# Kernel optimization log

Hardware: AMD Instinct MI355X
Metric: run time of the kernel (lower is better)

Reference implementation:

```python
import jax, jax.numpy as jnp
import numpy as np

B, T, C, H, S, M = 4, 4096, 1024, 16, 256, 32
D = C // H  # size_head = 64


def setup_inputs() -> dict:
    key = jax.random.key(0)
    ks = jax.random.split(key, 10)
    scale = 1.0 / (C * C)
    return {
        "x_q": jax.random.normal(ks[0], (B, T, C), dtype=jnp.float32),
        "x_r": jax.random.normal(ks[1], (B, T, C), dtype=jnp.float32),
        "y": jax.random.normal(ks[2], (B, T, C), dtype=jnp.float32),
        "Wi": jax.random.normal(ks[3], (C, C), dtype=jnp.float32) * 0.02,
        "bi": jnp.zeros((C,), jnp.float32),
        "Ws": jax.random.normal(ks[4], (S, D), dtype=jnp.float32) * 0.02,
        "bs": jnp.zeros((S,), jnp.float32),
        "temp": jnp.ones((1, H, 1, 1), jnp.float32) / jnp.sqrt(jnp.float32(D)),
        "w_re": jax.random.uniform(ks[5], (H, D, D, M), dtype=jnp.float32) * scale,
        "w_im": jax.random.uniform(ks[6], (H, D, D, M), dtype=jnp.float32) * scale,
        "Wo": jax.random.normal(ks[7], (C, C), dtype=jnp.float32) * 0.02,
        "bo": jnp.zeros((C,), jnp.float32),
    }


def reference(x_q, x_r, y, Wi, bi, Ws, bs, temp, w_re, w_im, Wo, bo):
    b, t, c = x_q.shape
    d = c // H
    # in_proj -> [B, H, T, D]
    tmp = (x_q @ Wi.T + bi).reshape(b, t, H, d).transpose(0, 2, 1, 3)
    # slice logits [B, H, T, S], scaled by learned temperature
    logits = (tmp @ Ws.T + bs) / temp
    # softmax over tokens (n): slice-attention pooling to S virtual points
    z = jnp.einsum('bhnc,bhns->bhsc', tmp, jax.nn.softmax(logits, axis=-2))
    z = z.transpose(0, 1, 3, 2)  # [B, H, D, S]
    n = z.shape[-1]
    z_fft = jnp.fft.rfft(z)  # [B, H, D, S//2+1]
    w = (w_re + 1j * w_im).astype(z_fft.dtype)
    out_m = jnp.einsum('bhix,hiox->bhox', z_fft[..., :M], w)  # [B, H, D, M]
    out_ft = jnp.zeros((b, H, d, n // 2 + 1), dtype=out_m.dtype).at[..., :M].set(out_m)
    out = jnp.fft.irfft(out_ft, n=n)  # [B, H, D, S]
    out = out.transpose(0, 1, 3, 2)  # [B, H, S, D]
    # softmax over slices (g): scatter back to tokens
    out = jnp.einsum('bhgc,bhng->bhnc', out, jax.nn.softmax(logits, axis=-1))
    out = out.transpose(0, 2, 1, 3).reshape(b, t, c)  # merge heads
    return out @ Wo.T + bo
```

## Files before the change

### kernel.cpp

```cpp
#include <hip/hip_runtime.h>
#include <hip/hip_bf16.h>

typedef __attribute__((ext_vector_type(8))) _Float16 half8;
typedef __attribute__((ext_vector_type(4))) _Float16 half4;
typedef __attribute__((ext_vector_type(4))) float f32x4;

#define DEVFN __device__ __forceinline__

constexpr int B_ = 4, T_ = 4096, C_ = 1024, H_ = 16, S_ = 256, M_ = 32, D_ = 64;
constexpr int NT_ = B_ * T_;
constexpr float FSCALE = 65536.0f;
constexpr float TWOPI = 6.283185307179586f;

DEVFN half8 cvt8(const float4 a, const float4 b) {
  half8 h;
  h[0] = (_Float16)a.x; h[1] = (_Float16)a.y; h[2] = (_Float16)a.z; h[3] = (_Float16)a.w;
  h[4] = (_Float16)b.x; h[5] = (_Float16)b.y; h[6] = (_Float16)b.z; h[7] = (_Float16)b.w;
  return h;
}

__global__ void k_diag(float* __restrict__ out, float wsz) {
  if (threadIdx.x == 0 && blockIdx.x == 0) out[0] = wsz;
}

__global__ void kw_cvt(const float* __restrict__ src, _Float16* __restrict__ dst, int n) {
  const int i = (blockIdx.x * blockDim.x + threadIdx.x) * 8;
  if (i < n) {
    float4 a = ((const float4*)(src + i))[0];
    float4 b = ((const float4*)(src + i))[1];
    *(half8*)(dst + i) = cvt8(a, b);
  }
}

__global__ void k0_prep(const float* __restrict__ Ws, const float* __restrict__ bs,
                        const float* __restrict__ temp,
                        _Float16* __restrict__ Wsh, float* __restrict__ bsh) {
  const int h = blockIdx.x;
  const int tid = threadIdx.x;
  const float invt = 1.0f / temp[h];
  for (int i = tid; i < S_ * D_; i += 256)
    Wsh[(size_t)h * S_ * D_ + i] = (_Float16)(Ws[i] * invt);
  if (tid < S_) bsh[h * S_ + tid] = bs[tid] * invt;
}

__global__ __launch_bounds__(256) void k1_in_proj(
    const float* __restrict__ X, const _Float16* __restrict__ Wih, const float* __restrict__ bi,
    _Float16* __restrict__ tmp_h)
{
  __shared__ _Float16 As[128][40];
  __shared__ _Float16 Bs[128][40];
  const int tid = threadIdx.x;
  const int orig = blockIdx.y * gridDim.x + blockIdx.x;
  const int wgid = (orig & 7) * 128 + (orig >> 3);
  const int rowBase = (wgid >> 3) * 128;
  const int colBase = (wgid & 7) * 128;
  const int w = tid >> 6, lane = tid & 63;
  const int wr = w >> 1, wc = w & 1;
  const int fr = lane & 15, fg = lane >> 4;
  const int sr = tid >> 1, sk = (tid & 1) * 16;
  f32x4 acc[4][4] = {};
  for (int kt = 0; kt < C_; kt += 32) {
    __syncthreads();
    {
      const float* s0 = X + (size_t)(rowBase + sr) * C_ + kt + sk;
      float4 v0 = ((const float4*)s0)[0], v1 = ((const float4*)s0)[1];
      float4 v2 = ((const float4*)s0)[2], v3 = ((const float4*)s0)[3];
      *(half8*)&As[sr][sk]     = cvt8(v0, v1);
      *(half8*)&As[sr][sk + 8] = cvt8(v2, v3);
      const _Float16* s1 = Wih + (size_t)(colBase + sr) * C_ + kt + sk;
      *(half8*)&Bs[sr][sk]     = ((const half8*)s1)[0];
      *(half8*)&Bs[sr][sk + 8] = ((const half8*)s1)[1];
    }
    __syncthreads();
    half8 a[4], b[4];
#pragma unroll
    for (int i = 0; i < 4; ++i) a[i] = *(const half8*)&As[wr * 64 + i * 16 + fr][fg * 8];
#pragma unroll
    for (int j = 0; j < 4; ++j) b[j] = *(const half8*)&Bs[wc * 64 + j * 16 + fr][fg * 8];
#pragma unroll
    for (int i = 0; i < 4; ++i)
#pragma unroll
      for (int j = 0; j < 4; ++j)
        acc[i][j] = __builtin_amdgcn_mfma_f32_16x16x32_f16(a[i], b[j], acc[i][j], 0, 0, 0);
  }
#pragma unroll
  for (int i = 0; i < 4; ++i) {
#pragma unroll
    for (int j = 0; j < 4; ++j) {
      const int col = colBase + wc * 64 + j * 16 + fr;
      const int hh = col >> 6, d = col & 63;
      const float bv = bi[col];
      const int g0 = rowBase + wr * 64 + i * 16 + fg * 4;
#pragma unroll
      for (int r = 0; r < 4; ++r) {
        const int g = g0 + r;
        const int bb = g >> 12;
        const int t = g & (T_ - 1);
        tmp_h[(((size_t)(bb * H_ + hh)) * T_ + t) * D_ + d] = (_Float16)(acc[i][j][r] + bv);
      }
    }
  }
}

__global__ __launch_bounds__(256) void k3_pool(
    const _Float16* __restrict__ tmp_h, const _Float16* __restrict__ Wsh,
    const float* __restrict__ bsh,
    float* __restrict__ Zpart, float* __restrict__ rowsum, float* __restrict__ colsumP)
{
  __shared__ _Float16 Es[256][72];
  __shared__ _Float16 Bt[64][72];
  __shared__ float red[64][4];
  const int tid = threadIdx.x;
  const int kc = blockIdx.x;
  const int bh = blockIdx.y;
  const int hh = bh & (H_ - 1);
  const int w = tid >> 6, lane = tid & 63;
  const int fr = lane & 15, fg = lane >> 4;
  const size_t tmpB = (size_t)bh * T_ * D_;
  const _Float16* WshH = Wsh + (size_t)hh * S_ * D_;
  float bsreg[4];
#pragma unroll
  for (int nj = 0; nj < 4; ++nj) bsreg[nj] = bsh[hh * S_ + w * 64 + nj * 16 + fr];
  f32x4 acc2[4][4] = {};
  float cacc[4] = {0.f, 0.f, 0.f, 0.f};
  for (int step = 0; step < 16; ++step) {
    const int t0 = kc * 1024 + step * 64;
    {
      const int tl = tid >> 2, cc = (tid & 3) * 16;
      const _Float16* src = tmp_h + tmpB + (size_t)(t0 + tl) * D_ + cc;
      half8 v0 = ((const half8*)src)[0];
      half8 v1 = ((const half8*)src)[1];
#pragma unroll
      for (int k2 = 0; k2 < 8; ++k2) Bt[cc + k2][tl] = v0[k2];
#pragma unroll
      for (int k2 = 0; k2 < 8; ++k2) Bt[cc + 8 + k2][tl] = v1[k2];
    }
    f32x4 acc1[4][4] = {};
#pragma unroll
    for (int ks = 0; ks < 2; ++ks) {
      half8 a[4], b[4];
#pragma unroll
      for (int mi = 0; mi < 4; ++mi)
        a[mi] = *(const half8*)(tmp_h + tmpB + (size_t)(t0 + mi * 16 + fr) * D_ + ks * 32 + fg * 8);
#pragma unroll
      for (int nj = 0; nj < 4; ++nj)
        b[nj] = *(const half8*)(WshH + (size_t)(w * 64 + nj * 16 + fr) * D_ + ks * 32 + fg * 8);
#pragma unroll
      for (int mi = 0; mi < 4; ++mi)
#pragma unroll
        for (int nj = 0; nj < 4; ++nj)
          acc1[mi][nj] = __builtin_amdgcn_mfma_f32_16x16x32_f16(a[mi], b[nj], acc1[mi][nj], 0, 0, 0);
    }
#pragma unroll
    for (int mi = 0; mi < 4; ++mi) {
      float rsp[4] = {0.f, 0.f, 0.f, 0.f};
#pragma unroll
      for (int nj = 0; nj < 4; ++nj) {
        half4 p;
        float csp = 0.f;
#pragma unroll
        for (int r = 0; r < 4; ++r) {
          const float e = __expf(acc1[mi][nj][r] + bsreg[nj]);
          p[r] = (_Float16)e;
          rsp[r] += e;
          csp += e;
        }
        cacc[nj] += csp;
        *(half4*)&Es[w * 64 + nj * 16 + fr][mi * 16 + fg * 4] = p;
      }
#pragma unroll
      for (int r = 0; r < 4; ++r) {
        float v = rsp[r];
        v += __shfl_xor(v, 1); v += __shfl_xor(v, 2);
        v += __shfl_xor(v, 4); v += __shfl_xor(v, 8);
        if (fr == 0) red[mi * 16 + fg * 4 + r][w] = v;
      }
    }
    __syncthreads();
#pragma unroll
    for (int kt = 0; kt < 2; ++kt) {
      half8 a2[4], b2[4];
#pragma unroll
      for (int mi = 0; mi < 4; ++mi) a2[mi] = *(const half8*)&Es[w * 64 + mi * 16 + fr][kt * 32 + fg * 8];
#pragma unroll
      for (int nj = 0; nj < 4; ++nj) b2[nj] = *(const half8*)&Bt[nj * 16 + fr][kt * 32 + fg * 8];
#pragma unroll
      for (int mi = 0; mi < 4; ++mi)
#pragma unroll
        for (int nj = 0; nj < 4; ++nj)
          acc2[mi][nj] = __builtin_amdgcn_mfma_f32_16x16x32_f16(a2[mi], b2[nj], acc2[mi][nj], 0, 0, 0);
    }
    if (tid < 64)
      rowsum[(size_t)bh * T_ + t0 + tid] = red[tid][0] + red[tid][1] + red[tid][2] + red[tid][3];
    __syncthreads();
  }
#pragma unroll
  for (int nj = 0; nj < 4; ++nj) {
    float v = cacc[nj];
    v += __shfl_xor(v, 16); v += __shfl_xor(v, 32);
    if (fg == 0) colsumP[((size_t)bh * 4 + kc) * S_ + w * 64 + nj * 16 + fr] = v;
  }
#pragma unroll
  for (int mi = 0; mi < 4; ++mi)
#pragma unroll
    for (int nj = 0; nj < 4; ++nj)
#pragma unroll
      for (int r = 0; r < 4; ++r)
        Zpart[(((size_t)bh * 4 + kc) * S_ + w * 64 + mi * 16 + fg * 4 + r) * D_ + nj * 16 + fr]
            = acc2[mi][nj][r];
}

__global__ __launch_bounds__(256) void k4a_dft(
    const float* __restrict__ Zpart, const float* __restrict__ colsumP,
    float* __restrict__ Fre, float* __restrict__ Fim)
{
  __shared__ float zsh[256][17];
  __shared__ float csh[256];
  __shared__ float tc[256], ts[256];
  const int tid = threadIdx.x;
  const int ic = blockIdx.x;
  const int bh = blockIdx.y;
  {
    const float ang = (float)tid * (TWOPI / 256.0f);
    tc[tid] = cosf(ang); ts[tid] = sinf(ang);
    float c = 0.f;
#pragma unroll
    for (int kc = 0; kc < 4; ++kc) c += colsumP[((size_t)bh * 4 + kc) * S_ + tid];
    csh[tid] = c;
  }
  __syncthreads();
  for (int idx = tid; idx < 256 * 16; idx += 256) {
    const int s = idx >> 4, dd = idx & 15;
    float v = 0.f;
#pragma unroll
    for (int kc = 0; kc < 4; ++kc)
      v += Zpart[(((size_t)bh * 4 + kc) * S_ + s) * D_ + ic * 16 + dd];
    zsh[s][dd] = v / csh[s];
  }
  __syncthreads();
  const int ii = tid >> 4;
  const int mh = tid & 15;
#pragma unroll
  for (int q = 0; q < 2; ++q) {
    const int m = mh + 16 * q;
    float re = 0.f, im = 0.f;
    int k = 0;
    for (int s = 0; s < 256; ++s) {
      const float zv = zsh[s][ii];
      re += zv * tc[k];
      im -= zv * ts[k];
      k = (k + m) & 255;
    }
    Fre[((size_t)bh * D_ + ic * 16 + ii) * M_ + m] = re;
    Fim[((size_t)bh * D_ + ic * 16 + ii) * M_ + m] = im;
  }
}

__global__ __launch_bounds__(256) void k4b_mix(
    const float* __restrict__ Fre, const float* __restrict__ Fim,
    const float* __restrict__ w_re, const float* __restrict__ w_im,
    _Float16* __restrict__ fout_T)
{
  __shared__ _Float16 Fsr[4][64][33];
  __shared__ _Float16 Fsi[4][64][33];
  __shared__ float Gpre[2][4][4][32];
  __shared__ float Gpim[2][4][4][32];
  __shared__ float Gre[4][4][32];
  __shared__ float Gim[4][4][32];
  __shared__ float tc[256], ts[256];
  const int tid = threadIdx.x;
  const int oc = blockIdx.x;
  const int h  = blockIdx.y;
  for (int idx = tid; idx < 4 * 64 * 32; idx += 256) {
    const int b = idx >> 11, rem = idx & 2047, i = rem >> 5, m = rem & 31;
    const size_t off = ((size_t)(b * 16 + h) * D_ + i) * M_ + m;
    Fsr[b][i][m] = (_Float16)Fre[off];
    Fsi[b][i][m] = (_Float16)Fim[off];
  }
  {
    const float ang = (float)tid * (TWOPI / 256.0f);
    tc[tid] = cosf(ang); ts[tid] = sinf(ang);
  }
  __syncthreads();
  {
    const int ih = tid >> 7, o = (tid >> 5) & 3, m = tid & 31;
    float gre[4] = {0,0,0,0}, gim[4] = {0,0,0,0};
    for (int i = ih * 32; i < ih * 32 + 32; ++i) {
      const size_t wo = (((size_t)h * D_ + i) * D_ + oc * 4 + o) * M_ + m;
      const float wre = w_re[wo], wim = w_im[wo];
#pragma unroll
      for (int b = 0; b < 4; ++b) {
        const float fre = (float)Fsr[b][i][m], fim = (float)Fsi[b][i][m];
        gre[b] += fre * wre - fim * wim;
        gim[b] += fre * wim + fim * wre;
      }
    }
#pragma unroll
    for (int b = 0; b < 4; ++b) { Gpre[ih][b][o][m] = gre[b]; Gpim[ih][b][o][m] = gim[b]; }
  }
  __syncthreads();
  for (int idx = tid; idx < 512; idx += 256) {
    const int b = idx >> 7, o = (idx >> 5) & 3, m = idx & 31;
    Gre[b][o][m] = Gpre[0][b][o][m] + Gpre[1][b][o][m];
    Gim[b][o][m] = Gpim[0][b][o][m] + Gpim[1][b][o][m];
  }
  __syncthreads();
  {
    const int b = tid >> 6, o = (tid >> 4) & 3, sc = tid & 15;
    for (int s5 = 0; s5 < 16; ++s5) {
      const int s = sc * 16 + s5;
      float v = Gre[b][o][0];
      int km = s;
#pragma unroll
      for (int m = 1; m < 32; ++m) {
        v += 2.0f * (Gre[b][o][m] * tc[km] - Gim[b][o][m] * ts[km]);
        km = (km + s) & 255;
      }
      fout_T[((size_t)(b * 16 + h) * D_ + oc * 4 + o) * S_ + s] = (_Float16)(v * (FSCALE / 256.0f));
    }
  }
}

__global__ __launch_bounds__(256) void k5_scatter(
    const _Float16* __restrict__ Wsh, const float* __restrict__ bsh,
    const _Float16* __restrict__ fout_T, const float* __restrict__ rowsum,
    _Float16* __restrict__ tmp_io)
{
  __shared__ _Float16 Fs[64][264];
  __shared__ _Float16 Es[64][264];
  __shared__ float bshl[256];
  const int tid = threadIdx.x;
  const int orig = blockIdx.y * gridDim.x + blockIdx.x;
  const int nidx = (orig & 7) * 64 + (orig >> 3);
  const int bh = nidx >> 3;
  const int tcn = nidx & 7;
  const int hh = bh & (H_ - 1);
  const int w = tid >> 6, lane = tid & 63;
  const int fr = lane & 15, fg = lane >> 4;
  {
    const int row = tid >> 2, c0 = (tid & 3) * 64;
    const _Float16* src = fout_T + (size_t)bh * D_ * S_ + (size_t)row * S_ + c0;
#pragma unroll
    for (int q = 0; q < 8; ++q)
      *(half8*)&Fs[row][c0 + q * 8] = ((const half8*)src)[q];
  }
  bshl[tid] = bsh[hh * S_ + tid];
  __syncthreads();
  const _Float16* WshH = Wsh + (size_t)hh * S_ * D_;
  const size_t tmpB = (size_t)bh * T_ * D_ + (size_t)tcn * 512 * D_;
  const int trow = w * 16 + fr;
  half8 bf0, bf1;
  {
    const _Float16* p = tmp_io + tmpB + (size_t)trow * D_ + fg * 8;
    bf0 = *(const half8*)p;
    bf1 = *(const half8*)(p + 32);
  }
  for (int step = 0; step < 8; ++step) {
    {
      f32x4 acc1[8];
#pragma unroll
      for (int mi = 0; mi < 8; ++mi) acc1[mi] = (f32x4){0.f, 0.f, 0.f, 0.f};
#pragma unroll
      for (int mi = 0; mi < 8; ++mi) {
        const half8 a0 = *(const half8*)(WshH + (size_t)(mi * 16 + fr) * D_ + fg * 8);
        acc1[mi] = __builtin_amdgcn_mfma_f32_16x16x32_f16(a0, bf0, acc1[mi], 0, 0, 0);
      }
#pragma unroll
      for (int mi = 0; mi < 8; ++mi) {
        const half8 a1 = *(const half8*)(WshH + (size_t)(mi * 16 + fr) * D_ + 32 + fg * 8);
        acc1[mi] = __builtin_amdgcn_mfma_f32_16x16x32_f16(a1, bf1, acc1[mi], 0, 0, 0);
      }
#pragma unroll
      for (int mi = 0; mi < 8; ++mi) {
        const float4 bv = *(const float4*)&bshl[mi * 16 + fg * 4];
        half4 pk;
        pk[0] = (_Float16)__expf(acc1[mi][0] + bv.x);
        pk[1] = (_Float16)__expf(acc1[mi][1] + bv.y);
        pk[2] = (_Float16)__expf(acc1[mi][2] + bv.z);
        pk[3] = (_Float16)__expf(acc1[mi][3] + bv.w);
        *(half4*)&Es[trow][mi * 16 + fg * 4] = pk;
      }
    }
    {
      f32x4 acc1[8];
#pragma unroll
      for (int mi = 0; mi < 8; ++mi) acc1[mi] = (f32x4){0.f, 0.f, 0.f, 0.f};
#pragma unroll
      for (int mi = 0; mi < 8; ++mi) {
        const half8 a0 = *(const half8*)(WshH + (size_t)((8 + mi) * 16 + fr) * D_ + fg * 8);
        acc1[mi] = __builtin_amdgcn_mfma_f32_16x16x32_f16(a0, bf0, acc1[mi], 0, 0, 0);
      }
#pragma unroll
      for (int mi = 0; mi < 8; ++mi) {
        const half8 a1 = *(const half8*)(WshH + (size_t)((8 + mi) * 16 + fr) * D_ + 32 + fg * 8);
        acc1[mi] = __builtin_amdgcn_mfma_f32_16x16x32_f16(a1, bf1, acc1[mi], 0, 0, 0);
      }
#pragma unroll
      for (int mi = 0; mi < 8; ++mi) {
        const float4 bv = *(const float4*)&bshl[(8 + mi) * 16 + fg * 4];
        half4 pk;
        pk[0] = (_Float16)__expf(acc1[mi][0] + bv.x);
        pk[1] = (_Float16)__expf(acc1[mi][1] + bv.y);
        pk[2] = (_Float16)__expf(acc1[mi][2] + bv.z);
        pk[3] = (_Float16)__expf(acc1[mi][3] + bv.w);
        *(half4*)&Es[trow][(8 + mi) * 16 + fg * 4] = pk;
      }
    }
    if (step < 7) {
      const _Float16* p = tmp_io + tmpB + (size_t)((step + 1) * 64 + trow) * D_ + fg * 8;
      bf0 = *(const half8*)p;
      bf1 = *(const half8*)(p + 32);
    }
    f32x4 acc2[4];
#pragma unroll
    for (int nj = 0; nj < 4; ++nj) acc2[nj] = (f32x4){0.f, 0.f, 0.f, 0.f};
#pragma unroll
    for (int ks = 0; ks < 8; ++ks) {
      const half8 ea = *(const half8*)&Es[w * 16 + fr][ks * 32 + fg * 8];
#pragma unroll
      for (int nj = 0; nj < 4; ++nj) {
        const half8 fb = *(const half8*)&Fs[nj * 16 + fr][ks * 32 + fg * 8];
        acc2[nj] = __builtin_amdgcn_mfma_f32_16x16x32_f16(ea, fb, acc2[nj], 0, 0, 0);
      }
    }
    const int tbase = tcn * 512 + step * 64 + w * 16 + fg * 4;
    const float4 rs = *(const float4*)&rowsum[(size_t)bh * T_ + tbase];
    const float ri[4] = {1.0f / rs.x, 1.0f / rs.y, 1.0f / rs.z, 1.0f / rs.w};
#pragma unroll
    for (int r = 0; r < 4; ++r) {
      _Float16* dst = tmp_io + (size_t)bh * T_ * D_ + (size_t)(tbase + r) * D_ + fr;
#pragma unroll
      for (int nj = 0; nj < 4; ++nj)
        dst[nj * 16] = (_Float16)(acc2[nj][r] * ri[r]);
    }
  }
}

__global__ __launch_bounds__(256) void k6_out_proj(
    const _Float16* __restrict__ OT, const _Float16* __restrict__ Woh, const float* __restrict__ bo,
    float* __restrict__ Y)
{
  __shared__ _Float16 As[128][40];
  __shared__ _Float16 Bs[128][40];
  const int tid = threadIdx.x;
  const int orig = blockIdx.y * gridDim.x + blockIdx.x;
  const int wgid = (orig & 7) * 128 + (orig >> 3);
  const int rowBase = (wgid >> 3) * 128;
  const int colBase = (wgid & 7) * 128;
  const int w = tid >> 6, lane = tid & 63;
  const int wr = w >> 1, wc = w & 1;
  const int fr = lane & 15, fg = lane >> 4;
  const int sr = tid >> 1, sk = (tid & 1) * 16;
  const int g = rowBase + sr;
  const int bb = g >> 12, t = g & (T_ - 1);
  f32x4 acc[4][4] = {};
  for (int kt = 0; kt < C_; kt += 32) {
    __syncthreads();
    {
      const int k0 = kt + sk;
      const int hh0 = k0 >> 6, d0 = k0 & 63;
      const _Float16* s0 = OT + (((size_t)(bb * H_ + hh0)) * T_ + t) * D_ + d0;
      *(half8*)&As[sr][sk]     = ((const half8*)s0)[0];
      *(half8*)&As[sr][sk + 8] = ((const half8*)s0)[1];
      const _Float16* s1 = Woh + (size_t)(colBase + sr) * C_ + kt + sk;
      *(half8*)&Bs[sr][sk]     = ((const half8*)s1)[0];
      *(half8*)&Bs[sr][sk + 8] = ((const half8*)s1)[1];
    }
    __syncthreads();
    half8 a[4], b[4];
#pragma unroll
    for (int i = 0; i < 4; ++i) a[i] = *(const half8*)&As[wr * 64 + i * 16 + fr][fg * 8];
#pragma unroll
    for (int j = 0; j < 4; ++j) b[j] = *(const half8*)&Bs[wc * 64 + j * 16 + fr][fg * 8];
#pragma unroll
    for (int i = 0; i < 4; ++i)
#pragma unroll
      for (int j = 0; j < 4; ++j)
        acc[i][j] = __builtin_amdgcn_mfma_f32_16x16x32_f16(a[i], b[j], acc[i][j], 0, 0, 0);
  }
#pragma unroll
  for (int i = 0; i < 4; ++i) {
#pragma unroll
    for (int j = 0; j < 4; ++j) {
      const int col = colBase + wc * 64 + j * 16 + fr;
      const float bv = bo[col];
      const int g0 = rowBase + wr * 64 + i * 16 + fg * 4;
#pragma unroll
      for (int r = 0; r < 4; ++r)
        Y[(size_t)(g0 + r) * C_ + col] = acc[i][j][r] * (1.0f / FSCALE) + bv;
    }
  }
}

extern "C" void kernel_launch(void* const* d_in, const int* in_sizes, int n_in,
                              void* d_out, int out_size, void* d_ws, size_t ws_size,
                              hipStream_t stream)
{
  const float* x_q  = (const float*)d_in[0];
  const float* Wi   = (const float*)d_in[3];
  const float* bi   = (const float*)d_in[4];
  const float* Ws   = (const float*)d_in[5];
  const float* bs   = (const float*)d_in[6];
  const float* temp = (const float*)d_in[7];
  const float* w_re = (const float*)d_in[8];
  const float* w_im = (const float*)d_in[9];
  const float* Wo   = (const float*)d_in[10];
  const float* bo   = (const float*)d_in[11];
  float* Y = (float*)d_out;

  char* ws = (char*)d_ws;
  size_t off = 0;
  auto alloc = [&](size_t bytes) { size_t o = off; off += (bytes + 255) & ~(size_t)255; return o; };
  const size_t o_tmp  = alloc((size_t)NT_ * C_ * 2);
  const size_t o_Wsh  = alloc((size_t)H_ * S_ * D_ * 2);
  const size_t o_bsh  = alloc((size_t)H_ * S_ * 4);
  const size_t o_Zp   = alloc((size_t)B_ * H_ * 4 * S_ * D_ * 4);
  const size_t o_row  = alloc((size_t)B_ * H_ * T_ * 4);
  const size_t o_colP = alloc((size_t)B_ * H_ * 4 * S_ * 4);
  const size_t o_Fre  = alloc((size_t)B_ * H_ * D_ * M_ * 4);
  const size_t o_Fim  = alloc((size_t)B_ * H_ * D_ * M_ * 4);
  const size_t o_fout = alloc((size_t)B_ * H_ * D_ * S_ * 2);
  const size_t o_Wih  = alloc((size_t)C_ * C_ * 2);
  const size_t o_Woh  = alloc((size_t)C_ * C_ * 2);
  if (off > ws_size) {
    k_diag<<<1, 64, 0, stream>>>(Y, (float)ws_size);
    return;
  }

  _Float16* tmp    = (_Float16*)(ws + o_tmp);
  _Float16* Wsh    = (_Float16*)(ws + o_Wsh);
  float*    bsh    = (float*)(ws + o_bsh);
  float*    Zpart  = (float*)(ws + o_Zp);
  float*    rowsum = (float*)(ws + o_row);
  float*    colsumP= (float*)(ws + o_colP);
  float*    Fre    = (float*)(ws + o_Fre);
  float*    Fim    = (float*)(ws + o_Fim);
  _Float16* fout_T = (_Float16*)(ws + o_fout);
  _Float16* Wih    = (_Float16*)(ws + o_Wih);
  _Float16* Woh    = (_Float16*)(ws + o_Woh);

  kw_cvt    <<<dim3(512),     256, 0, stream>>>(Wi, Wih, C_ * C_);
  kw_cvt    <<<dim3(512),     256, 0, stream>>>(Wo, Woh, C_ * C_);
  k0_prep   <<<dim3(H_),      256, 0, stream>>>(Ws, bs, temp, Wsh, bsh);
  k1_in_proj<<<dim3(8, 128),  256, 0, stream>>>(x_q, Wih, bi, tmp);
  k3_pool   <<<dim3(4, B_*H_), 256, 0, stream>>>(tmp, Wsh, bsh, Zpart, rowsum, colsumP);
  k4a_dft   <<<dim3(4, B_*H_), 256, 0, stream>>>(Zpart, colsumP, Fre, Fim);
  k4b_mix   <<<dim3(16, H_),   256, 0, stream>>>(Fre, Fim, w_re, w_im, fout_T);
  k5_scatter<<<dim3(8, B_*H_), 256, 0, stream>>>(Wsh, bsh, fout_T, rowsum, tmp);
  k6_out_proj<<<dim3(8, 128),  256, 0, stream>>>(tmp, Woh, bo, Y);
}
```

Baseline: 338.7 us.

## Load GEMM tiles directly into LDS and pre-convert activations to fp16

Both projection GEMMs now stage their A and B tiles with global_load_lds (direct global-to-LDS 16-byte loads) into unpadded 32-wide LDS rows instead of going through registers. To make this possible for the input projection, x_q is first converted to fp16 by a separate kernel into the output buffer, which is used as scratch. This removes register staging and the per-tile float conversion inside the GEMM, at the cost of an extra full pass over x_q. Dropping the padding may also introduce LDS bank conflicts on the fragment reads.

```diff
diff --git a/kernel.cpp b/kernel.cpp
--- a/kernel.cpp
+++ b/kernel.cpp
@@ -18,6 +18,11 @@
   h[4] = (_Float16)b.x; h[5] = (_Float16)b.y; h[6] = (_Float16)b.z; h[7] = (_Float16)b.w;
   return h;
 }
+
+#define GLD16(gsrc, ldst)                                                        \
+  __builtin_amdgcn_global_load_lds(                                              \
+      (const __attribute__((address_space(1))) uint32_t*)(gsrc),                 \
+      (__attribute__((address_space(3))) uint32_t*)(ldst), 16, 0, 0)
 
 __global__ void k_diag(float* __restrict__ out, float wsz) {
   if (threadIdx.x == 0 && blockIdx.x == 0) out[0] = wsz;
@@ -44,11 +49,11 @@
 }
 
 __global__ __launch_bounds__(256) void k1_in_proj(
-    const float* __restrict__ X, const _Float16* __restrict__ Wih, const float* __restrict__ bi,
+    const _Float16* __restrict__ Xh, const _Float16* __restrict__ Wih, const float* __restrict__ bi,
     _Float16* __restrict__ tmp_h)
 {
-  __shared__ _Float16 As[128][40];
-  __shared__ _Float16 Bs[128][40];
+  __shared__ _Float16 As[128 * 32];
+  __shared__ _Float16 Bs[128 * 32];
   const int tid = threadIdx.x;
   const int orig = blockIdx.y * gridDim.x + blockIdx.x;
   const int wgid = (orig & 7) * 128 + (orig >> 3);
@@ -57,26 +62,26 @@
   const int w = tid >> 6, lane = tid & 63;
   const int wr = w >> 1, wc = w & 1;
   const int fr = lane & 15, fg = lane >> 4;
-  const int sr = tid >> 1, sk = (tid & 1) * 16;
+  const int srow0 = w * 16 + (lane >> 2);
+  const int srow1 = (4 + w) * 16 + (lane >> 2);
+  const int scol  = (lane & 3) * 8;
+  const size_t arow0 = (size_t)(rowBase + srow0) * C_ + scol;
+  const size_t arow1 = (size_t)(rowBase + srow1) * C_ + scol;
+  const size_t brow0 = (size_t)(colBase + srow0) * C_ + scol;
+  const size_t brow1 = (size_t)(colBase + srow1) * C_ + scol;
   f32x4 acc[4][4] = {};
   for (int kt = 0; kt < C_; kt += 32) {
     __syncthreads();
-    {
-      const float* s0 = X + (size_t)(rowBase + sr) * C_ + kt + sk;
-      float4 v0 = ((const float4*)s0)[0], v1 = ((const float4*)s0)[1];
-      float4 v2 = ((const float4*)s0)[2], v3 = ((const float4*)s0)[3];
-      *(half8*)&As[sr][sk]     = cvt8(v0, v1);
-      *(half8*)&As[sr][sk + 8] = cvt8(v2, v3);
-      const _Float16* s1 = Wih + (size_t)(colBase + sr) * C_ + kt + sk;
-      *(half8*)&Bs[sr][sk]     = ((const half8*)s1)[0];
-      *(half8*)&Bs[sr][sk + 8] = ((const half8*)s1)[1];
-    }
+    GLD16(Xh  + arow0 + kt, &As[w * 512]);
+    GLD16(Xh  + arow1 + kt, &As[(4 + w) * 512]);
+    GLD16(Wih + brow0 + kt, &Bs[w * 512]);
+    GLD16(Wih + brow1 + kt, &Bs[(4 + w) * 512]);
     __syncthreads();
     half8 a[4], b[4];
 #pragma unroll
-    for (int i = 0; i < 4; ++i) a[i] = *(const half8*)&As[wr * 64 + i * 16 + fr][fg * 8];
-#pragma unroll
-    for (int j = 0; j < 4; ++j) b[j] = *(const half8*)&Bs[wc * 64 + j * 16 + fr][fg * 8];
+    for (int i = 0; i < 4; ++i) a[i] = *(const half8*)&As[(wr * 64 + i * 16 + fr) * 32 + fg * 8];
+#pragma unroll
+    for (int j = 0; j < 4; ++j) b[j] = *(const half8*)&Bs[(wc * 64 + j * 16 + fr) * 32 + fg * 8];
 #pragma unroll
     for (int i = 0; i < 4; ++i)
 #pragma unroll
@@ -440,8 +445,8 @@
     const _Float16* __restrict__ OT, const _Float16* __restrict__ Woh, const float* __restrict__ bo,
     float* __restrict__ Y)
 {
-  __shared__ _Float16 As[128][40];
-  __shared__ _Float16 Bs[128][40];
+  __shared__ _Float16 As[128 * 32];
+  __shared__ _Float16 Bs[128 * 32];
   const int tid = threadIdx.x;
   const int orig = blockIdx.y * gridDim.x + blockIdx.x;
   const int wgid = (orig & 7) * 128 + (orig >> 3);
@@ -450,28 +455,29 @@
   const int w = tid >> 6, lane = tid & 63;
   const int wr = w >> 1, wc = w & 1;
   const int fr = lane & 15, fg = lane >> 4;
-  const int sr = tid >> 1, sk = (tid & 1) * 16;
-  const int g = rowBase + sr;
-  const int bb = g >> 12, t = g & (T_ - 1);
+  const int srow0 = w * 16 + (lane >> 2);
+  const int srow1 = (4 + w) * 16 + (lane >> 2);
+  const int scol  = (lane & 3) * 8;
+  const int g0 = rowBase + srow0, g1 = rowBase + srow1;
+  const int bb = g0 >> 12;
+  const int t0 = g0 & (T_ - 1), t1 = g1 & (T_ - 1);
+  const size_t brow0 = (size_t)(colBase + srow0) * C_ + scol;
+  const size_t brow1 = (size_t)(colBase + srow1) * C_ + scol;
   f32x4 acc[4][4] = {};
   for (int kt = 0; kt < C_; kt += 32) {
+    const int c0 = kt + scol;
+    const int hh0 = c0 >> 6, d0 = c0 & 63;
     __syncthreads();
-    {
-      const int k0 = kt + sk;
-      const int hh0 = k0 >> 6, d0 = k0 & 63;
-      const _Float16* s0 = OT + (((size_t)(bb * H_ + hh0)) * T_ + t) * D_ + d0;
-      *(half8*)&As[sr][sk]     = ((const half8*)s0)[0];
-      *(half8*)&As[sr][sk + 8] = ((const half8*)s0)[1];
-      const _Float16* s1 = Woh + (size_t)(colBase + sr) * C_ + kt + sk;
-      *(half8*)&Bs[sr][sk]     = ((const half8*)s1)[0];
-      *(half8*)&Bs[sr][sk + 8] = ((const half8*)s1)[1];
-    }
+    GLD16(OT + (((size_t)(bb * H_ + hh0)) * T_ + t0) * D_ + d0, &As[w * 512]);
+    GLD16(OT + (((size_t)(bb * H_ + hh0)) * T_ + t1) * D_ + d0, &As[(4 + w) * 512]);
+    GLD16(Woh + brow0 + kt, &Bs[w * 512]);
+    GLD16(Woh + brow1 + kt, &Bs[(4 + w) * 512]);
     __syncthreads();
     half8 a[4], b[4];
 #pragma unroll
-    for (int i = 0; i < 4; ++i) a[i] = *(const half8*)&As[wr * 64 + i * 16 + fr][fg * 8];
-#pragma unroll
-    for (int j = 0; j < 4; ++j) b[j] = *(const half8*)&Bs[wc * 64 + j * 16 + fr][fg * 8];
+    for (int i = 0; i < 4; ++i) a[i] = *(const half8*)&As[(wr * 64 + i * 16 + fr) * 32 + fg * 8];
+#pragma unroll
+    for (int j = 0; j < 4; ++j) b[j] = *(const half8*)&Bs[(wc * 64 + j * 16 + fr) * 32 + fg * 8];
 #pragma unroll
     for (int i = 0; i < 4; ++i)
 #pragma unroll
@@ -484,10 +490,10 @@
     for (int j = 0; j < 4; ++j) {
       const int col = colBase + wc * 64 + j * 16 + fr;
       const float bv = bo[col];
-      const int g0 = rowBase + wr * 64 + i * 16 + fg * 4;
+      const int g0o = rowBase + wr * 64 + i * 16 + fg * 4;
 #pragma unroll
       for (int r = 0; r < 4; ++r)
-        Y[(size_t)(g0 + r) * C_ + col] = acc[i][j][r] * (1.0f / FSCALE) + bv;
+        Y[(size_t)(g0o + r) * C_ + col] = acc[i][j][r] * (1.0f / FSCALE) + bv;
     }
   }
 }
@@ -538,11 +544,13 @@
   _Float16* fout_T = (_Float16*)(ws + o_fout);
   _Float16* Wih    = (_Float16*)(ws + o_Wih);
   _Float16* Woh    = (_Float16*)(ws + o_Woh);
-
+  _Float16* Xh     = (_Float16*)d_out;
+
+  kw_cvt    <<<dim3(8192),    256, 0, stream>>>(x_q, Xh, NT_ * C_);
   kw_cvt    <<<dim3(512),     256, 0, stream>>>(Wi, Wih, C_ * C_);
   kw_cvt    <<<dim3(512),     256, 0, stream>>>(Wo, Woh, C_ * C_);
   k0_prep   <<<dim3(H_),      256, 0, stream>>>(Ws, bs, temp, Wsh, bsh);
-  k1_in_proj<<<dim3(8, 128),  256, 0, stream>>>(x_q, Wih, bi, tmp);
+  k1_in_proj<<<dim3(8, 128),  256, 0, stream>>>(Xh, Wih, bi, tmp);
   k3_pool   <<<dim3(4, B_*H_), 256, 0, stream>>>(tmp, Wsh, bsh, Zpart, rowsum, colsumP);
   k4a_dft   <<<dim3(4, B_*H_), 256, 0, stream>>>(Zpart, colsumP, Fre, Fim);
   k4b_mix   <<<dim3(16, H_),   256, 0, stream>>>(Fre, Fim, w_re, w_im, fout_T);
```

Measured after the change: 312.0 us. -7.9%, faster.
